# Kernel optimization log

Measured on AMD Instinct MI355X. Metric: run time of the kernel, lower is better.

The kernel has to match this reference:

```python
import jax, jax.numpy as jnp
import numpy as np

N, D, H = 100000, 128, 8
C = D // H
E = 800000
NEG_SLOPE = 0.2


def setup_inputs() -> dict:
    key = jax.random.key(0)
    k1, k2, k3, k4, k5, k6 = jax.random.split(key, 6)
    x = jax.random.normal(k1, (N, D), dtype=jnp.float32)
    edge_index = jax.random.randint(k2, (2, E), 0, N, dtype=jnp.int64)
    # GATConv params: shared linear (single node-feature input), per-head attention vectors, bias
    W = jax.random.normal(k3, (D, H * C), dtype=jnp.float32) * (1.0 / np.sqrt(D))
    att_src = jax.random.normal(k4, (H, C), dtype=jnp.float32) * 0.1
    att_dst = jax.random.normal(k5, (H, C), dtype=jnp.float32) * 0.1
    bias = jnp.zeros((H * C,), dtype=jnp.float32)
    return {"x": x, "edge_index": edge_index, "W": W, "att_src": att_src, "att_dst": att_dst, "bias": bias}


def reference(x, edge_index, W, att_src, att_dst, bias):
    # PyG GATConv default: add self-loops
    loops = jnp.tile(jnp.arange(N, dtype=edge_index.dtype), (2, 1))  # [2, N]
    ei = jnp.concatenate([edge_index, loops], axis=1)                # [2, E+N]
    src, dst = ei[0], ei[1]

    h = (x @ W).reshape(N, H, C)                    # [N, H, C]
    a_src = jnp.einsum('nhc,hc->nh', h, att_src)    # [N, H]
    a_dst = jnp.einsum('nhc,hc->nh', h, att_dst)    # [N, H]

    logits = jax.nn.leaky_relu(a_src[src] + a_dst[dst], negative_slope=NEG_SLOPE)  # [Etot, H]

    # segment softmax grouped by destination node (every node has a self-loop -> non-empty)
    mx = jax.ops.segment_max(logits, dst, num_segments=N)   # [N, H]
    ex = jnp.exp(logits - mx[dst])                           # [Etot, H]
    denom = jax.ops.segment_sum(ex, dst, num_segments=N)    # [N, H]
    alpha = ex / (denom[dst] + 1e-16)                        # [Etot, H]

    msg = h[src] * alpha[:, :, None]                         # [Etot, H, C]
    out = jax.ops.segment_sum(msg, dst, num_segments=N)      # [N, H, C]
    out = out.reshape(N, H * C) + bias                       # concat heads
    return out, ei, alpha
```

## Files before the change

kernel.cpp:

```cpp
#include <hip/hip_runtime.h>
#include <hip/hip_bf16.h>
#include <cstdint>

#define N_NODES 100000
#define DIM 128
#define HEADS 8
#define CH 16
#define NEDGE 800000
#define ETOT (NEDGE + N_NODES)
#define NEG_SLOPE 0.2f
#define CAP 64
#define PRE 16

typedef __attribute__((ext_vector_type(8))) short bf16x8;
typedef __attribute__((ext_vector_type(4))) float f32x4;

__device__ __forceinline__ float leaky(float v) {
    return v >= 0.f ? v : NEG_SLOPE * v;
}

__device__ __forceinline__ void wave_lds_fence() {
    asm volatile("s_waitcnt lgkmcnt(0)" ::: "memory");
    __builtin_amdgcn_sched_barrier(0);
}

__device__ __forceinline__ void split2(float w, ushort& hi, ushort& lo) {
    __hip_bfloat16 bh = __float2bfloat16(w);
    float r = w - __bfloat162float(bh);
    __hip_bfloat16 bl = __float2bfloat16(r);
    hi = *(ushort*)&bh;
    lo = *(ushort*)&bl;
}

#define NCOLS 144
#define LDK   136
#define MT    128

__global__ __launch_bounds__(512, 4) void gemm_kernel(
    const float* __restrict__ x, const float* __restrict__ W,
    const float* __restrict__ att_src, const float* __restrict__ att_dst,
    __hip_bfloat16* __restrict__ h, float* __restrict__ a_src,
    float* __restrict__ a_dst)
{
    __shared__ ushort Whi[NCOLS * LDK];
    __shared__ ushort Wlo[NCOLS * LDK];
    const int tid = threadIdx.x;

    {
        const int n  = tid >> 2;
        const int kq = (tid & 3) * 32;
        #pragma unroll
        for (int j = 0; j < 32; j += 2) {
            const int k = kq + j;
            float w0 = W[(size_t)k * DIM + n];
            float w1 = W[(size_t)(k + 1) * DIM + n];
            ushort h0, l0, h1, l1;
            split2(w0, h0, l0);
            split2(w1, h1, l1);
            *(uint*)&Whi[n * LDK + k] = (uint)h0 | ((uint)h1 << 16);
            *(uint*)&Wlo[n * LDK + k] = (uint)l0 | ((uint)l1 << 16);
        }
    }
    if (tid < 64) {
        const int t  = tid >> 2;
        const int kq = (tid & 3) * 32;
        const int hd = t & 7;
        const float* av = ((t < 8) ? att_src : att_dst) + hd * CH;
        float avr[CH];
        #pragma unroll
        for (int c = 0; c < CH; ++c) avr[c] = av[c];
        const int nrow = 128 + t;
        for (int j = 0; j < 32; j += 2) {
            const int k = kq + j;
            const float* wp0 = &W[(size_t)k * DIM + hd * CH];
            const float* wp1 = wp0 + DIM;
            float s0 = 0.f, s1 = 0.f;
            #pragma unroll
            for (int c = 0; c < CH; ++c) { s0 += wp0[c] * avr[c]; s1 += wp1[c] * avr[c]; }
            ushort h0, l0, h1, l1;
            split2(s0, h0, l0);
            split2(s1, h1, l1);
            *(uint*)&Whi[nrow * LDK + k] = (uint)h0 | ((uint)h1 << 16);
            *(uint*)&Wlo[nrow * LDK + k] = (uint)l0 | ((uint)l1 << 16);
        }
    }
    __syncthreads();

    const int w    = tid >> 6;
    const int lane = tid & 63;
    const int r    = lane & 15;
    const int g    = lane >> 4;
    const long arow = (long)blockIdx.x * MT + w * 16 + r;
    const bool avalid = arow < N_NODES;

    f32x4 acc[9] = {};
    #pragma unroll
    for (int ks = 0; ks < 4; ++ks) {
        const int k0 = ks * 32 + g * 8;
        float xv[8];
        if (avalid) {
            *(float4*)&xv[0] = *(const float4*)&x[arow * DIM + k0];
            *(float4*)&xv[4] = *(const float4*)&x[arow * DIM + k0 + 4];
        } else {
            #pragma unroll
            for (int j = 0; j < 8; ++j) xv[j] = 0.f;
        }
        bf16x8 ahi, alo;
        #pragma unroll
        for (int j = 0; j < 8; ++j) {
            ushort hb, lb;
            split2(xv[j], hb, lb);
            ahi[j] = (short)hb;
            alo[j] = (short)lb;
        }
        #pragma unroll
        for (int nt = 0; nt < 9; ++nt) {
            const int nr = nt * 16 + r;
            bf16x8 bhi = *(const bf16x8*)&Whi[nr * LDK + k0];
            bf16x8 blo = *(const bf16x8*)&Wlo[nr * LDK + k0];
            acc[nt] = __builtin_amdgcn_mfma_f32_16x16x32_bf16(ahi, bhi, acc[nt], 0, 0, 0);
            acc[nt] = __builtin_amdgcn_mfma_f32_16x16x32_bf16(alo, bhi, acc[nt], 0, 0, 0);
            acc[nt] = __builtin_amdgcn_mfma_f32_16x16x32_bf16(ahi, blo, acc[nt], 0, 0, 0);
        }
    }

    const long orow0 = (long)blockIdx.x * MT + w * 16 + g * 4;
    #pragma unroll
    for (int q = 0; q < 4; ++q) {
        const long orow = orow0 + q;
        if (orow < N_NODES) {
            #pragma unroll
            for (int nt = 0; nt < 8; ++nt)
                h[orow * DIM + nt * 16 + r] = __float2bfloat16(acc[nt][q]);
            const float av = acc[8][q];
            if (r < 8) a_src[orow * HEADS + r]       = av;
            else       a_dst[orow * HEADS + (r - 8)] = av;
        }
    }
}

__global__ __launch_bounds__(256) void edge_kernel(const int* __restrict__ edge_index,
                                                   float* __restrict__ ei_out,
                                                   int* __restrict__ fill,
                                                   int* __restrict__ ebuf) {
    int e = blockIdx.x * 256 + threadIdx.x;
    if (e >= ETOT) return;
    int s, d;
    if (e < NEDGE) { s = edge_index[e]; d = edge_index[NEDGE + e]; }
    else           { s = d = e - NEDGE; }
    ei_out[e]        = (float)s;
    ei_out[ETOT + e] = (float)d;
    int pos = atomicAdd(&fill[d], 1);
    if (pos < CAP) ebuf[d * CAP + pos] = e;
}

__global__ __launch_bounds__(256) void gather_kernel(const int* __restrict__ edge_index,
                                                     const int* __restrict__ fill,
                                                     const int* __restrict__ ebuf,
                                                     const __hip_bfloat16* __restrict__ h,
                                                     const float* __restrict__ a_src,
                                                     const float* __restrict__ a_dst,
                                                     const float* __restrict__ bias,
                                                     float* __restrict__ alpha_out,
                                                     float* __restrict__ out) {
    __shared__ int   s_s[4][CAP];
    __shared__ int   s_e[4][CAP];
    __shared__ float s_al[4][CAP][9];
    const int tid  = threadIdx.x;
    const int w    = tid >> 6;
    const int lane = tid & 63;
    const int n    = blockIdx.x * 4 + w;
    const int head = lane >> 3, c = lane & 7;
    const int chb  = head * CH + c * 2;
    const int dn   = min(fill[n], CAP);
    const float ad = a_dst[(uint)n * HEADS + head];

    if (lane < dn) {
        int e = ebuf[(uint)n * CAP + lane];
        s_e[w][lane] = e;
        s_s[w][lane] = (e < NEDGE) ? edge_index[e] : e - NEDGE;
    }
    wave_lds_fence();

    const char* hb  = (const char*)h;
    const uint  cho = (uint)chb * 2u;
    const int npre = min(dn, PRE);
    unsigned hv[PRE];
    #pragma unroll
    for (int q = 0; q < PRE; ++q) {
        if (q < npre)
            hv[q] = *(const unsigned*)(hb + ((uint)s_s[w][q] * 256u + cho));
    }

    const char* asb = (const char*)a_src;
    const uint  hdo = (uint)(head << 2);
    float m = -1e30f;
    for (int i = c; i < dn; i += 8) {
        float as = *(const float*)(asb + ((uint)s_s[w][i] * 32u + hdo));
        float lg = leaky(as + ad);
        s_al[w][i][head] = lg;
        m = fmaxf(m, lg);
    }
    #pragma unroll
    for (int off = 1; off < 8; off <<= 1)
        m = fmaxf(m, __shfl_xor(m, off));

    float dsum = 0.f;
    for (int i = c; i < dn; i += 8) {
        float ex = __expf(s_al[w][i][head] - m);
        s_al[w][i][head] = ex;
        dsum += ex;
    }
    #pragma unroll
    for (int off = 1; off < 8; off <<= 1)
        dsum += __shfl_xor(dsum, off);
    const float rdinv = 1.f / (dsum + 1e-16f);
    wave_lds_fence();

    float ax = 0.f, ay = 0.f;
    #pragma unroll
    for (int q = 0; q < PRE; ++q) {
        if (q < npre) {
            float ex = s_al[w][q][head];
            ax += __uint_as_float(hv[q] << 16) * ex;
            ay += __uint_as_float(hv[q] & 0xffff0000u) * ex;
        }
    }
    for (int i = PRE; i < dn; ++i) {
        unsigned hq = *(const unsigned*)(hb + ((uint)s_s[w][i] * 256u + cho));
        float ex = s_al[w][i][head];
        ax += __uint_as_float(hq << 16) * ex;
        ay += __uint_as_float(hq & 0xffff0000u) * ex;
    }
    ax *= rdinv; ay *= rdinv;
    float2 b = *(const float2*)&bias[chb];
    float2 r; r.x = ax + b.x; r.y = ay + b.y;
    *(float2*)&out[(uint)n * DIM + chb] = r;

    for (int i = c; i < dn; i += 8)
        alpha_out[(uint)s_e[w][i] * 8u + head] = s_al[w][i][head] * rdinv;
}

extern "C" void kernel_launch(void* const* d_in, const int* in_sizes, int n_in,
                              void* d_out, int out_size, void* d_ws, size_t ws_size,
                              hipStream_t stream) {
    const float* x          = (const float*)d_in[0];
    const int*   edge_index = (const int*)d_in[1];
    const float* W          = (const float*)d_in[2];
    const float* att_src    = (const float*)d_in[3];
    const float* att_dst    = (const float*)d_in[4];
    const float* bias       = (const float*)d_in[5];

    float* out       = (float*)d_out;
    float* ei_out    = out + (size_t)N_NODES * DIM;
    float* alpha_out = ei_out + 2 * (size_t)ETOT;

    __hip_bfloat16* h = (__hip_bfloat16*)d_ws;
    float* a_src = (float*)(h + (size_t)N_NODES * DIM);
    float* a_dst = a_src + (size_t)N_NODES * HEADS;
    int*   fill  = (int*)(a_dst + (size_t)N_NODES * HEADS);
    int*   ebuf  = fill + N_NODES;

    hipMemsetAsync(fill, 0, (size_t)N_NODES * sizeof(int), stream);

    edge_kernel<<<(ETOT + 255) / 256, 256, 0, stream>>>(edge_index, ei_out, fill, ebuf);
    gemm_kernel<<<(N_NODES + MT - 1) / MT, 512, 0, stream>>>(x, W, att_src, att_dst,
                                                             h, a_src, a_dst);
    gather_kernel<<<N_NODES / 4, 256, 0, stream>>>(edge_index, fill, ebuf, h,
                                                   a_src, a_dst, bias, alpha_out, out);
}
```

Baseline: 299.0 us.

## Fuse edge bucketing with GEMM launch and make gather kernel LDS-free via shuffles

The edge-bucketing and projection GEMM kernels are merged into one launch. The first blocks do the edge scatter and the rest do the GEMM, so the two independent stages can overlap and one launch is dropped. The gather kernel no longer stages source indices and logits in shared memory. It keeps them in registers and broadcasts them with wave shuffles, and for edges past the prefetch window it recomputes the exp instead of reading a stored value. It also raises the prefetch depth and sets an occupancy hint. Edge blocks now carry the GEMM's large LDS footprint, which may limit how many run at once, and the larger register arrays could increase register pressure.

```diff
diff --git a/kernel.cpp b/kernel.cpp
--- a/kernel.cpp
+++ b/kernel.cpp
@@ -10,18 +10,13 @@
 #define ETOT (NEDGE + N_NODES)
 #define NEG_SLOPE 0.2f
 #define CAP 64
-#define PRE 16
+#define PRE 20
 
 typedef __attribute__((ext_vector_type(8))) short bf16x8;
 typedef __attribute__((ext_vector_type(4))) float f32x4;
 
 __device__ __forceinline__ float leaky(float v) {
     return v >= 0.f ? v : NEG_SLOPE * v;
-}
-
-__device__ __forceinline__ void wave_lds_fence() {
-    asm volatile("s_waitcnt lgkmcnt(0)" ::: "memory");
-    __builtin_amdgcn_sched_barrier(0);
 }
 
 __device__ __forceinline__ void split2(float w, ushort& hi, ushort& lo) {
@@ -35,16 +30,36 @@
 #define NCOLS 144
 #define LDK   136
 #define MT    128
-
-__global__ __launch_bounds__(512, 4) void gemm_kernel(
+#define EDGE_TPB 512
+#define EDGE_BLOCKS ((ETOT + EDGE_TPB - 1) / EDGE_TPB)
+#define GEMM_BLOCKS ((N_NODES + MT - 1) / MT)
+
+__global__ __launch_bounds__(512, 4) void fused_kernel(
     const float* __restrict__ x, const float* __restrict__ W,
     const float* __restrict__ att_src, const float* __restrict__ att_dst,
     __hip_bfloat16* __restrict__ h, float* __restrict__ a_src,
-    float* __restrict__ a_dst)
+    float* __restrict__ a_dst,
+    const int* __restrict__ edge_index, float* __restrict__ ei_out,
+    int* __restrict__ fill, int* __restrict__ ebuf)
 {
     __shared__ ushort Whi[NCOLS * LDK];
     __shared__ ushort Wlo[NCOLS * LDK];
     const int tid = threadIdx.x;
+
+    if (blockIdx.x < EDGE_BLOCKS) {
+        const int e = blockIdx.x * EDGE_TPB + tid;
+        if (e < ETOT) {
+            int s, d;
+            if (e < NEDGE) { s = edge_index[e]; d = edge_index[NEDGE + e]; }
+            else           { s = d = e - NEDGE; }
+            ei_out[e]        = (float)s;
+            ei_out[ETOT + e] = (float)d;
+            int pos = atomicAdd(&fill[d], 1);
+            if (pos < CAP) ebuf[d * CAP + pos] = e;
+        }
+        return;
+    }
+    const int bid = blockIdx.x - EDGE_BLOCKS;
 
     {
         const int n  = tid >> 2;
@@ -90,7 +105,7 @@
     const int lane = tid & 63;
     const int r    = lane & 15;
     const int g    = lane >> 4;
-    const long arow = (long)blockIdx.x * MT + w * 16 + r;
+    const long arow = (long)bid * MT + w * 16 + r;
     const bool avalid = arow < N_NODES;
 
     f32x4 acc[9] = {};
@@ -124,7 +139,7 @@
         }
     }
 
-    const long orow0 = (long)blockIdx.x * MT + w * 16 + g * 4;
+    const long orow0 = (long)bid * MT + w * 16 + g * 4;
     #pragma unroll
     for (int q = 0; q < 4; ++q) {
         const long orow = orow0 + q;
@@ -139,48 +154,24 @@
     }
 }
 
-__global__ __launch_bounds__(256) void edge_kernel(const int* __restrict__ edge_index,
-                                                   float* __restrict__ ei_out,
-                                                   int* __restrict__ fill,
-                                                   int* __restrict__ ebuf) {
-    int e = blockIdx.x * 256 + threadIdx.x;
-    if (e >= ETOT) return;
-    int s, d;
-    if (e < NEDGE) { s = edge_index[e]; d = edge_index[NEDGE + e]; }
-    else           { s = d = e - NEDGE; }
-    ei_out[e]        = (float)s;
-    ei_out[ETOT + e] = (float)d;
-    int pos = atomicAdd(&fill[d], 1);
-    if (pos < CAP) ebuf[d * CAP + pos] = e;
-}
-
-__global__ __launch_bounds__(256) void gather_kernel(const int* __restrict__ edge_index,
-                                                     const int* __restrict__ fill,
-                                                     const int* __restrict__ ebuf,
-                                                     const __hip_bfloat16* __restrict__ h,
-                                                     const float* __restrict__ a_src,
-                                                     const float* __restrict__ a_dst,
-                                                     const float* __restrict__ bias,
-                                                     float* __restrict__ alpha_out,
-                                                     float* __restrict__ out) {
-    __shared__ int   s_s[4][CAP];
-    __shared__ int   s_e[4][CAP];
-    __shared__ float s_al[4][CAP][9];
+__global__ __launch_bounds__(256, 8) void gather_kernel(
+    const int* __restrict__ edge_index, const int* __restrict__ fill,
+    const int* __restrict__ ebuf, const __hip_bfloat16* __restrict__ h,
+    const float* __restrict__ a_src, const float* __restrict__ a_dst,
+    const float* __restrict__ bias, float* __restrict__ alpha_out,
+    float* __restrict__ out)
+{
     const int tid  = threadIdx.x;
-    const int w    = tid >> 6;
     const int lane = tid & 63;
-    const int n    = blockIdx.x * 4 + w;
+    const int n    = blockIdx.x * 4 + (tid >> 6);
     const int head = lane >> 3, c = lane & 7;
     const int chb  = head * CH + c * 2;
-    const int dn   = min(fill[n], CAP);
+
+    const int   dn = min(fill[n], CAP);
     const float ad = a_dst[(uint)n * HEADS + head];
-
-    if (lane < dn) {
-        int e = ebuf[(uint)n * CAP + lane];
-        s_e[w][lane] = e;
-        s_s[w][lane] = (e < NEDGE) ? edge_index[e] : e - NEDGE;
-    }
-    wave_lds_fence();
+    const int   e  = ebuf[(uint)n * CAP + lane];
+    int s = 0;
+    if (lane < dn) s = (e < NEDGE) ? edge_index[e] : e - NEDGE;
 
     const char* hb  = (const char*)h;
     const uint  cho = (uint)chb * 2u;
@@ -188,57 +179,71 @@
     unsigned hv[PRE];
     #pragma unroll
     for (int q = 0; q < PRE; ++q) {
+        int sq = __shfl(s, q);
         if (q < npre)
-            hv[q] = *(const unsigned*)(hb + ((uint)s_s[w][q] * 256u + cho));
+            hv[q] = *(const unsigned*)(hb + ((uint)sq * 256u + cho));
     }
 
     const char* asb = (const char*)a_src;
     const uint  hdo = (uint)(head << 2);
+    float lg[8];
     float m = -1e30f;
-    for (int i = c; i < dn; i += 8) {
-        float as = *(const float*)(asb + ((uint)s_s[w][i] * 32u + hdo));
-        float lg = leaky(as + ad);
-        s_al[w][i][head] = lg;
-        m = fmaxf(m, lg);
+    #pragma unroll
+    for (int k = 0; k < 8; ++k) {
+        const int i = c + 8 * k;
+        if (i < dn) {
+            int si = __shfl(s, i);
+            float as = *(const float*)(asb + ((uint)si * 32u + hdo));
+            lg[k] = leaky(as + ad);
+            m = fmaxf(m, lg[k]);
+        }
     }
     #pragma unroll
     for (int off = 1; off < 8; off <<= 1)
         m = fmaxf(m, __shfl_xor(m, off));
 
+    float ex[8];
     float dsum = 0.f;
-    for (int i = c; i < dn; i += 8) {
-        float ex = __expf(s_al[w][i][head] - m);
-        s_al[w][i][head] = ex;
-        dsum += ex;
+    #pragma unroll
+    for (int k = 0; k < 8; ++k) {
+        const int i = c + 8 * k;
+        if (i < dn) { ex[k] = __expf(lg[k] - m); dsum += ex[k]; }
     }
     #pragma unroll
     for (int off = 1; off < 8; off <<= 1)
         dsum += __shfl_xor(dsum, off);
     const float rdinv = 1.f / (dsum + 1e-16f);
-    wave_lds_fence();
 
     float ax = 0.f, ay = 0.f;
     #pragma unroll
     for (int q = 0; q < PRE; ++q) {
         if (q < npre) {
-            float ex = s_al[w][q][head];
-            ax += __uint_as_float(hv[q] << 16) * ex;
-            ay += __uint_as_float(hv[q] & 0xffff0000u) * ex;
-        }
-    }
-    for (int i = PRE; i < dn; ++i) {
-        unsigned hq = *(const unsigned*)(hb + ((uint)s_s[w][i] * 256u + cho));
-        float ex = s_al[w][i][head];
-        ax += __uint_as_float(hq << 16) * ex;
-        ay += __uint_as_float(hq & 0xffff0000u) * ex;
+            float exq = __shfl(ex[q >> 3], head * 8 + (q & 7));
+            ax += __uint_as_float(hv[q] << 16) * exq;
+            ay += __uint_as_float(hv[q] & 0xffff0000u) * exq;
+        }
+    }
+    for (int q = PRE; q < dn; ++q) {
+        int sq = __shfl(s, q);
+        unsigned hq = *(const unsigned*)(hb + ((uint)sq * 256u + cho));
+        float asq = *(const float*)(asb + ((uint)sq * 32u + hdo));
+        float exq = __expf(leaky(asq + ad) - m);
+        ax += __uint_as_float(hq << 16) * exq;
+        ay += __uint_as_float(hq & 0xffff0000u) * exq;
     }
     ax *= rdinv; ay *= rdinv;
     float2 b = *(const float2*)&bias[chb];
-    float2 r; r.x = ax + b.x; r.y = ay + b.y;
-    *(float2*)&out[(uint)n * DIM + chb] = r;
-
-    for (int i = c; i < dn; i += 8)
-        alpha_out[(uint)s_e[w][i] * 8u + head] = s_al[w][i][head] * rdinv;
+    float2 rr; rr.x = ax + b.x; rr.y = ay + b.y;
+    *(float2*)&out[(uint)n * DIM + chb] = rr;
+
+    #pragma unroll
+    for (int k = 0; k < 8; ++k) {
+        const int i = c + 8 * k;
+        if (i < dn) {
+            int ei = __shfl(e, i);
+            alpha_out[(uint)ei * 8u + head] = ex[k] * rdinv;
+        }
+    }
 }
 
 extern "C" void kernel_launch(void* const* d_in, const int* in_sizes, int n_in,
@@ -263,9 +268,9 @@
 
     hipMemsetAsync(fill, 0, (size_t)N_NODES * sizeof(int), stream);
 
-    edge_kernel<<<(ETOT + 255) / 256, 256, 0, stream>>>(edge_index, ei_out, fill, ebuf);
-    gemm_kernel<<<(N_NODES + MT - 1) / MT, 512, 0, stream>>>(x, W, att_src, att_dst,
-                                                             h, a_src, a_dst);
+    fused_kernel<<<EDGE_BLOCKS + GEMM_BLOCKS, 512, 0, stream>>>(
+        x, W, att_src, att_dst, h, a_src, a_dst,
+        edge_index, ei_out, fill, ebuf);
     gather_kernel<<<N_NODES / 4, 256, 0, stream>>>(edge_index, fill, ebuf, h,
                                                    a_src, a_dst, bias, alpha_out, out);
 }
```

New measurement: 292.9 us. 2.0% less time.

## Fuse edge bucketing into GEMM kernel to overlap with W staging

Applied to the files above, without the earlier changes.

Merges the edge-scatter kernel into the GEMM kernel. Each 512-thread block processes 1536 edges: it loads the indices, writes ei_out and issues the fill atomics before W preparation, then writes ebuf before the barrier. This removes one kernel launch and lets edge memory traffic overlap with GEMM weight staging and compute. The cost is higher register pressure and longer per-block latency in the GEMM.

```diff
diff --git a/kernel.cpp b/kernel.cpp
--- a/kernel.cpp
+++ b/kernel.cpp
@@ -35,16 +35,41 @@
 #define NCOLS 144
 #define LDK   136
 #define MT    128
-
-__global__ __launch_bounds__(512, 4) void gemm_kernel(
+#define GEMM_BLOCKS ((N_NODES + MT - 1) / MT)
+#define EPB  1536
+
+__global__ __launch_bounds__(512, 4) void fused_kernel(
     const float* __restrict__ x, const float* __restrict__ W,
     const float* __restrict__ att_src, const float* __restrict__ att_dst,
     __hip_bfloat16* __restrict__ h, float* __restrict__ a_src,
-    float* __restrict__ a_dst)
+    float* __restrict__ a_dst,
+    const int* __restrict__ edge_index, float* __restrict__ ei_out,
+    int* __restrict__ fill, int* __restrict__ ebuf)
 {
     __shared__ ushort Whi[NCOLS * LDK];
     __shared__ ushort Wlo[NCOLS * LDK];
     const int tid = threadIdx.x;
+    const int bid = blockIdx.x;
+
+    int ee[3], es[3], ed[3];
+    #pragma unroll
+    for (int t = 0; t < 3; ++t) {
+        const int e = bid * EPB + t * 512 + tid;
+        ee[t] = e;
+        if (e < ETOT) {
+            if (e < NEDGE) { es[t] = edge_index[e]; ed[t] = edge_index[NEDGE + e]; }
+            else           { es[t] = ed[t] = e - NEDGE; }
+        }
+    }
+    int pos[3];
+    #pragma unroll
+    for (int t = 0; t < 3; ++t) {
+        if (ee[t] < ETOT) {
+            ei_out[ee[t]]        = (float)es[t];
+            ei_out[ETOT + ee[t]] = (float)ed[t];
+            pos[t] = atomicAdd(&fill[ed[t]], 1);
+        }
+    }
 
     {
         const int n  = tid >> 2;
@@ -84,13 +109,19 @@
             *(uint*)&Wlo[nrow * LDK + k] = (uint)l0 | ((uint)l1 << 16);
         }
     }
+
+    #pragma unroll
+    for (int t = 0; t < 3; ++t) {
+        if (ee[t] < ETOT && pos[t] < CAP)
+            ebuf[ed[t] * CAP + pos[t]] = ee[t];
+    }
     __syncthreads();
 
     const int w    = tid >> 6;
     const int lane = tid & 63;
     const int r    = lane & 15;
     const int g    = lane >> 4;
-    const long arow = (long)blockIdx.x * MT + w * 16 + r;
+    const long arow = (long)bid * MT + w * 16 + r;
     const bool avalid = arow < N_NODES;
 
     f32x4 acc[9] = {};
@@ -124,7 +155,7 @@
         }
     }
 
-    const long orow0 = (long)blockIdx.x * MT + w * 16 + g * 4;
+    const long orow0 = (long)bid * MT + w * 16 + g * 4;
     #pragma unroll
     for (int q = 0; q < 4; ++q) {
         const long orow = orow0 + q;
@@ -139,30 +170,13 @@
     }
 }
 
-__global__ __launch_bounds__(256) void edge_kernel(const int* __restrict__ edge_index,
-                                                   float* __restrict__ ei_out,
-                                                   int* __restrict__ fill,
-                                                   int* __restrict__ ebuf) {
-    int e = blockIdx.x * 256 + threadIdx.x;
-    if (e >= ETOT) return;
-    int s, d;
-    if (e < NEDGE) { s = edge_index[e]; d = edge_index[NEDGE + e]; }
-    else           { s = d = e - NEDGE; }
-    ei_out[e]        = (float)s;
-    ei_out[ETOT + e] = (float)d;
-    int pos = atomicAdd(&fill[d], 1);
-    if (pos < CAP) ebuf[d * CAP + pos] = e;
-}
-
-__global__ __launch_bounds__(256) void gather_kernel(const int* __restrict__ edge_index,
-                                                     const int* __restrict__ fill,
-                                                     const int* __restrict__ ebuf,
-                                                     const __hip_bfloat16* __restrict__ h,
-                                                     const float* __restrict__ a_src,
-                                                     const float* __restrict__ a_dst,
-                                                     const float* __restrict__ bias,
-                                                     float* __restrict__ alpha_out,
-                                                     float* __restrict__ out) {
+__global__ __launch_bounds__(256) void gather_kernel(
+    const int* __restrict__ edge_index, const int* __restrict__ fill,
+    const int* __restrict__ ebuf, const __hip_bfloat16* __restrict__ h,
+    const float* __restrict__ a_src, const float* __restrict__ a_dst,
+    const float* __restrict__ bias, float* __restrict__ alpha_out,
+    float* __restrict__ out)
+{
     __shared__ int   s_s[4][CAP];
     __shared__ int   s_e[4][CAP];
     __shared__ float s_al[4][CAP][9];
@@ -263,9 +277,9 @@
 
     hipMemsetAsync(fill, 0, (size_t)N_NODES * sizeof(int), stream);
 
-    edge_kernel<<<(ETOT + 255) / 256, 256, 0, stream>>>(edge_index, ei_out, fill, ebuf);
-    gemm_kernel<<<(N_NODES + MT - 1) / MT, 512, 0, stream>>>(x, W, att_src, att_dst,
-                                                             h, a_src, a_dst);
+    fused_kernel<<<GEMM_BLOCKS, 512, 0, stream>>>(
+        x, W, att_src, att_dst, h, a_src, a_dst,
+        edge_index, ei_out, fill, ebuf);
     gather_kernel<<<N_NODES / 4, 256, 0, stream>>>(edge_index, fill, ebuf, h,
                                                    a_src, a_dst, bias, alpha_out, out);
 }
```

Measured after the change: 277.8 us. 1.08x faster.
